# Kernel optimization log

Measured on AMD Instinct MI355X. Metric: run time of the kernel, lower is better.

## Reference

```python
import jax, jax.numpy as jnp
import numpy as np

RADIUS = 0.2
NSAMPLE = 32
NPOINT = 2048
EPS = 1e-5


def setup_inputs() -> dict:
    key = jax.random.key(0)
    ks = jax.random.split(key, 6)
    B, N, C = 8, 8192, 64
    xyz = jax.random.uniform(ks[0], (B, N, 3), dtype=jnp.float32)
    features = jax.random.normal(ks[1], (B, C, N), dtype=jnp.float32)
    W1 = jax.random.normal(ks[2], (64, 67), dtype=jnp.float32) * 0.1
    W2 = jax.random.normal(ks[3], (64, 64), dtype=jnp.float32) * 0.1
    W3 = jax.random.normal(ks[4], (128, 64), dtype=jnp.float32) * 0.1
    return {
        'xyz': xyz, 'features': features,
        'W1': W1, 'g1': jnp.ones((64,), jnp.float32), 'b1': jnp.zeros((64,), jnp.float32),
        'W2': W2, 'g2': jnp.ones((64,), jnp.float32), 'b2': jnp.zeros((64,), jnp.float32),
        'W3': W3, 'g3': jnp.ones((128,), jnp.float32), 'b3': jnp.zeros((128,), jnp.float32),
    }


def furthest_point_sample(xyz, npoint):
    # xyz: (B, N, 3) -> (B, npoint) int32 indices, first index is 0 (CUDA FPS convention)
    B, N, _ = xyz.shape
    idxs0 = jnp.zeros((B, npoint), dtype=jnp.int32)
    dists0 = jnp.full((B, N), 1e10, dtype=xyz.dtype)
    last0 = jnp.zeros((B,), dtype=jnp.int32)

    def body(i, state):
        idxs, dists, last = state
        last_pt = xyz[jnp.arange(B), last]                      # (B, 3)
        d = jnp.sum((xyz - last_pt[:, None, :]) ** 2, axis=-1)  # (B, N)
        dists = jnp.minimum(dists, d)
        nxt = jnp.argmax(dists, axis=-1).astype(jnp.int32)
        idxs = idxs.at[:, i].set(nxt)
        return (idxs, dists, nxt)

    idxs, _, _ = jax.lax.fori_loop(1, npoint, body, (idxs0, dists0, last0))
    return idxs


def ball_query(xyz, new_xyz, radius, nsample):
    # Returns (B, S, nsample) int32: first `nsample` points within radius of each
    # query center, padded with the first in-ball index (pointnet2 convention).
    N = xyz.shape[1]
    d2 = jnp.sum((new_xyz[:, :, None, :] - xyz[:, None, :, :]) ** 2, axis=-1)  # (B,S,N)
    key = jnp.where(d2 < radius * radius, jnp.arange(N, dtype=jnp.int32), N)
    neg_vals, _ = jax.lax.top_k(-key, nsample)   # k smallest keys = earliest in-ball indices
    cand = -neg_vals                             # (B, S, nsample)
    first = cand[..., :1]
    return jnp.where(cand < N, cand, first)


def reference(xyz, features, W1, g1, b1, W2, g2, b2, W3, g3, b3):
    B = xyz.shape[0]
    fps_idx = furthest_point_sample(xyz, NPOINT)              # (B, S)
    new_xyz = xyz[jnp.arange(B)[:, None], fps_idx]            # (B, S, 3)

    idx = ball_query(xyz, new_xyz, RADIUS, NSAMPLE)           # (B, S, ns)
    bb = jnp.arange(B)[:, None, None]
    grouped_xyz = xyz[bb, idx] - new_xyz[:, :, None, :]       # (B, S, ns, 3) relative coords
    grouped_f = features.transpose(0, 2, 1)[bb, idx]          # (B, S, ns, C)
    g = jnp.concatenate([grouped_xyz, grouped_f], axis=-1)    # (B, S, ns, 3+C)
    g = g.transpose(0, 3, 1, 2)                               # (B, 3+C, S, ns)

    for W, ga, be in ((W1, g1, b1), (W2, g2, b2), (W3, g3, b3)):
        h = jnp.einsum('oc,bcsn->bosn', W, g)                 # 1x1 conv
        mu = h.mean(axis=(0, 2, 3), keepdims=True)            # training-mode BN stats
        var = h.var(axis=(0, 2, 3), keepdims=True)
        h = (h - mu) / jnp.sqrt(var + EPS)
        g = jax.nn.relu(h * ga[None, :, None, None] + be[None, :, None, None])

    feats = g.max(axis=-1)                                    # (B, mlp[-1], S)
    return new_xyz, feats
```

## Files before the change

### kernel.cpp

```cpp
#include <hip/hip_runtime.h>
#include <hip/hip_bf16.h>
#include <stdint.h>

#define NB 8
#define NN 8192
#define NC 64
#define NS 2048
#define NK 32
#define NCOL (NB*NS*NK)

typedef float v2f __attribute__((ext_vector_type(2)));

__device__ __forceinline__ unsigned short f2bf(float x) {
    union { float f; unsigned u; } c; c.f = x;
    unsigned r = c.u + 0x7fffu + ((c.u >> 16) & 1u);
    return (unsigned short)(r >> 16);
}
__device__ __forceinline__ float bf2f(unsigned v16) {
    union { float f; unsigned u; } c; c.u = v16 << 16;
    return c.f;
}

template<int CTRL>
__device__ __forceinline__ unsigned long long dpp_max_u64(unsigned long long key) {
    int olo = __builtin_amdgcn_update_dpp(0, (int)(unsigned)key,        CTRL, 0xf, 0xf, true);
    int ohi = __builtin_amdgcn_update_dpp(0, (int)(unsigned)(key >> 32), CTRL, 0xf, 0xf, true);
    unsigned long long ok = ((unsigned long long)(unsigned)ohi << 32) | (unsigned)olo;
    return ok > key ? ok : key;
}
template<int CTRL>
__device__ __forceinline__ float dpp_add_f32(float x) {
    int o = __builtin_amdgcn_update_dpp(0, __float_as_int(x), CTRL, 0xf, 0xf, true);
    return x + __int_as_float(o);
}
template<int CTRL>
__device__ __forceinline__ float dpp_max_f32(float x) {
    int o = __builtin_amdgcn_update_dpp(__float_as_int(x), __float_as_int(x), CTRL, 0xf, 0xf, false);
    return fmaxf(x, __int_as_float(o));
}
template<int CTRL>
__device__ __forceinline__ float dpp_min_f32(float x) {
    int o = __builtin_amdgcn_update_dpp(__float_as_int(x), __float_as_int(x), CTRL, 0xf, 0xf, false);
    return fminf(x, __int_as_float(o));
}
template<int CTRL, int RM>
__device__ __forceinline__ unsigned dpp_add_u32(unsigned x) {
    int o = __builtin_amdgcn_update_dpp(0, (int)x, CTRL, RM, 0xf, true);
    return x + (unsigned)o;
}
__device__ __forceinline__ float wave_red_min(float x) {
    x = dpp_min_f32<0x111>(x); x = dpp_min_f32<0x112>(x);
    x = dpp_min_f32<0x114>(x); x = dpp_min_f32<0x118>(x);
    x = dpp_min_f32<0x142>(x); x = dpp_min_f32<0x143>(x);
    return __int_as_float(__builtin_amdgcn_readlane(__float_as_int(x), 63));
}
__device__ __forceinline__ float wave_red_max(float x) {
    x = dpp_max_f32<0x111>(x); x = dpp_max_f32<0x112>(x);
    x = dpp_max_f32<0x114>(x); x = dpp_max_f32<0x118>(x);
    x = dpp_max_f32<0x142>(x); x = dpp_max_f32<0x143>(x);
    return __int_as_float(__builtin_amdgcn_readlane(__float_as_int(x), 63));
}
__device__ __forceinline__ v2f relu2(v2f v) {
    v.x = fmaxf(v.x, 0.f); v.y = fmaxf(v.y, 0.f); return v;
}

__device__ __forceinline__ unsigned expand_bits10(unsigned v) {
    v = (v * 0x00010001u) & 0xFF0000FFu;
    v = (v * 0x00000101u) & 0x0F00F00Fu;
    v = (v * 0x00000011u) & 0xC30C30C3u;
    v = (v * 0x00000005u) & 0x49249249u;
    return v;
}
__global__ __launch_bounds__(1024) void sort_kernel(const float* __restrict__ xyz,
    float4* __restrict__ sorted)
{
    __shared__ unsigned cnt[2048];
    __shared__ unsigned codes[NN];
    __shared__ unsigned wsum[16];
    const int b = blockIdx.x;
    const int tid = threadIdx.x;
    const int w = tid >> 6;
    const int lane = tid & 63;
    const float* xb = xyz + (size_t)b * NN * 3;
    cnt[tid] = 0; cnt[tid + 1024] = 0;
    __syncthreads();
    for (int p = tid; p < NN; p += 1024) {
        float x = xb[3*p+0], y = xb[3*p+1], z = xb[3*p+2];
        int qx = (int)(x * 1024.f); qx = qx < 0 ? 0 : (qx > 1023 ? 1023 : qx);
        int qy = (int)(y * 1024.f); qy = qy < 0 ? 0 : (qy > 1023 ? 1023 : qy);
        int qz = (int)(z * 1024.f); qz = qz < 0 ? 0 : (qz > 1023 ? 1023 : qz);
        unsigned m = expand_bits10((unsigned)qx)
                   | (expand_bits10((unsigned)qy) << 1)
                   | (expand_bits10((unsigned)qz) << 2);
        unsigned bk = m >> 19;
        codes[p] = bk;
        atomicAdd(&cnt[bk], 1u);
    }
    __syncthreads();
    unsigned c0 = cnt[2*tid], c1 = cnt[2*tid+1];
    unsigned s = c0 + c1;
    unsigned v = s;
    v = dpp_add_u32<0x111, 0xf>(v);
    v = dpp_add_u32<0x112, 0xf>(v);
    v = dpp_add_u32<0x114, 0xf>(v);
    v = dpp_add_u32<0x118, 0xf>(v);
    v = dpp_add_u32<0x142, 0xa>(v);
    v = dpp_add_u32<0x143, 0xc>(v);
    if (lane == 63) wsum[w] = v;
    __syncthreads();
    unsigned wbase = 0;
#pragma unroll
    for (int j = 0; j < 15; ++j) {
        unsigned t = wsum[j];
        wbase += (j < w) ? t : 0u;
    }
    unsigned excl = wbase + v - s;
    cnt[2*tid]   = excl;
    cnt[2*tid+1] = excl + c0;
    __syncthreads();
    for (int p = tid; p < NN; p += 1024) {
        unsigned bk = codes[p];
        unsigned pos = atomicAdd(&cnt[bk], 1u);
        float4 o;
        o.x = xb[3*p+0]; o.y = xb[3*p+1]; o.z = xb[3*p+2];
        o.w = __int_as_float(p);
        sorted[(size_t)b * NN + pos] = o;
    }
}

__global__ __launch_bounds__(1024) void fps_kernel(const float* __restrict__ xyz,
    const float4* __restrict__ sorted,
    float* __restrict__ new_xyz, float* __restrict__ out_newxyz)
{
#pragma clang fp contract(off)
    const int b = blockIdx.x;
    const int tid = threadIdx.x;
    const int w = tid >> 6;
    const int lane = tid & 63;
    __shared__ float sx[NN], sy[NN], sz[NN];
    __shared__ float s_hist[NS * 3];
    __shared__ unsigned long long s_key[16];
    const float4* sp = sorted + (size_t)b * NN + (size_t)w * 512 + lane;
    v2f px[4], py[4], pz[4], dmin[4];
    unsigned plo[8];
    float bnx = 1e30f, bny = 1e30f, bnz = 1e30f;
    float bxx = -1e30f, bxy = -1e30f, bxz = -1e30f;
#pragma unroll
    for (int m = 0; m < 4; ++m) {
        float4 a = sp[128*m];
        float4 c = sp[128*m + 64];
        px[m].x = a.x; px[m].y = c.x;
        py[m].x = a.y; py[m].y = c.y;
        pz[m].x = a.z; pz[m].y = c.z;
        dmin[m].x = 1e10f; dmin[m].y = 1e10f;
        int ia = __float_as_int(a.w), ic = __float_as_int(c.w);
        plo[2*m]   = ~(unsigned)ia;
        plo[2*m+1] = ~(unsigned)ic;
        sx[ia] = a.x; sy[ia] = a.y; sz[ia] = a.z;
        sx[ic] = c.x; sy[ic] = c.y; sz[ic] = c.z;
        bnx = fminf(bnx, fminf(a.x, c.x)); bxx = fmaxf(bxx, fmaxf(a.x, c.x));
        bny = fminf(bny, fminf(a.y, c.y)); bxy = fmaxf(bxy, fmaxf(a.y, c.y));
        bnz = fminf(bnz, fminf(a.z, c.z)); bxz = fmaxf(bxz, fmaxf(a.z, c.z));
    }
    bnx = wave_red_min(bnx); bny = wave_red_min(bny); bnz = wave_red_min(bnz);
    bxx = wave_red_max(bxx); bxy = wave_red_max(bxy); bxz = wave_red_max(bxz);

    const float* xb = xyz + (size_t)b * NN * 3;
    float lx = xb[0], ly = xb[1], lz = xb[2];
    if (tid == 0) { s_hist[0] = lx; s_hist[1] = ly; s_hist[2] = lz; }
    float ckv = 1e30f;
    unsigned cklo = 0u;
    __syncthreads();

    for (int i = 1; i < NS; ++i) {
        float cdx = fmaxf(fmaxf(bnx - lx, lx - bxx), 0.f);
        float cdy = fmaxf(fmaxf(bny - ly, ly - bxy), 0.f);
        float cdz = fmaxf(fmaxf(bnz - lz, lz - bxz), 0.f);
        float lb = (cdx*cdx + cdy*cdy) + cdz*cdz;
        if (!(lb >= ckv)) {
            v2f l2x; l2x.x = lx; l2x.y = lx;
            v2f l2y; l2y.x = ly; l2y.y = ly;
            v2f l2z; l2z.x = lz; l2z.y = lz;
            unsigned long long best = 0ull;
#pragma unroll
            for (int m = 0; m < 4; ++m) {
                v2f dx = px[m] - l2x;
                v2f dy = py[m] - l2y;
                v2f dz = pz[m] - l2z;
                v2f d = (dx*dx + dy*dy) + dz*dz;
                v2f dm;
                dm.x = fminf(dmin[m].x, d.x);
                dm.y = fminf(dmin[m].y, d.y);
                dmin[m] = dm;
                unsigned long long k0 =
                    ((unsigned long long)__float_as_uint(dm.x) << 32) | plo[2*m];
                unsigned long long k1 =
                    ((unsigned long long)__float_as_uint(dm.y) << 32) | plo[2*m+1];
                if (k0 > best) best = k0;
                if (k1 > best) best = k1;
            }
            best = dpp_max_u64<0x111>(best);
            best = dpp_max_u64<0x112>(best);
            best = dpp_max_u64<0x114>(best);
            best = dpp_max_u64<0x118>(best);
            best = dpp_max_u64<0x142>(best);
            best = dpp_max_u64<0x143>(best);
            ckv  = __uint_as_float((unsigned)__builtin_amdgcn_readlane((int)(best >> 32), 63));
            cklo = (unsigned)__builtin_amdgcn_readlane((int)(best & 0xffffffffull), 63);
        }
        if (lane == 0)
            s_key[w] = ((unsigned long long)__float_as_uint(ckv) << 32) | cklo;
        __syncthreads();
        if (w == 0) {
            unsigned long long k = s_key[lane & 15];
            k = dpp_max_u64<0x111>(k);
            k = dpp_max_u64<0x112>(k);
            k = dpp_max_u64<0x114>(k);
            k = dpp_max_u64<0x118>(k);
            int lo15 = __builtin_amdgcn_readlane((int)(k & 0xffffffffull), 15);
            int ix = ~lo15;
            float nx = sx[ix], ny = sy[ix], nz = sz[ix];
            if (lane == 0) {
                s_hist[3*i+0] = nx; s_hist[3*i+1] = ny; s_hist[3*i+2] = nz;
            }
        }
        __syncthreads();
        lx = s_hist[3*i+0]; ly = s_hist[3*i+1]; lz = s_hist[3*i+2];
    }
    __syncthreads();
    float* nw = new_xyz + (size_t)b * NS * 3;
    float* ow = out_newxyz + (size_t)b * NS * 3;
    for (int t = tid; t < NS * 3; t += 1024) {
        float v = s_hist[t];
        nw[t] = v; ow[t] = v;
    }
}

__global__ __launch_bounds__(256) void transpose_kernel(const float* __restrict__ f,
    float* __restrict__ ft)
{
    __shared__ float tile[64][65];
    int b = blockIdx.y;
    int p0 = blockIdx.x * 64;
    for (int k = threadIdx.x; k < 64*64; k += 256) {
        int c = k >> 6, p = k & 63;
        tile[c][p] = f[((size_t)b * NC + c) * NN + p0 + p];
    }
    __syncthreads();
    for (int k = threadIdx.x; k < 64*64; k += 256) {
        int p = k >> 6, c = k & 63;
        ft[((size_t)b * NN + p0 + p) * NC + c] = tile[c][p];
    }
}

__global__ __launch_bounds__(256) void ballquery_kernel(const float* __restrict__ xyz,
    const float* __restrict__ new_xyz, int* __restrict__ idx)
{
#pragma clang fp contract(off)
    const int q = blockIdx.x * 4 + (threadIdx.x >> 6);
    const int lane = threadIdx.x & 63;
    const int b = q >> 11;
    const float r2 = (float)(0.2 * 0.2);
    const float* xb = xyz + (size_t)b * NN * 3;
    const float* nx = new_xyz + (size_t)q * 3;
    float qx = nx[0], qy = nx[1], qz = nx[2];
    int cnt = 0, first = -1;
    int* out = idx + (size_t)q * NK;
    for (int base = 0; base < NN; base += 64) {
        int p = base + lane;
        float x = xb[p*3+0], y = xb[p*3+1], z = xb[p*3+2];
        float dx = qx - x, dy = qy - y, dz = qz - z;
        float d2 = (dx*dx + dy*dy) + dz*dz;
        bool in = d2 < r2;
        unsigned long long m = __ballot(in);
        if (m) {
            if (first < 0) first = base + __builtin_ctzll(m);
            if (in) {
                int rank = cnt + __popcll(m & ((1ull << lane) - 1ull));
                if (rank < NK) out[rank] = p;
            }
            cnt += __popcll(m);
            if (cnt >= NK) break;
        }
    }
    for (int k = cnt + lane; k < NK; k += 64) out[k] = first;
}

__global__ __launch_bounds__(256, 2) void layer1_kernel(const float* __restrict__ xyz,
    const float* __restrict__ new_xyz, const int* __restrict__ idx,
    const float* __restrict__ ft, const float* __restrict__ W1,
    unsigned short* __restrict__ h1)
{
    const int col = blockIdx.x * 256 + threadIdx.x;
    const int b = col >> 16;
    const int s = (col >> 5) & 2047;
    const int p = idx[col];
    v2f g[34];
    float* gf = (float*)g;
    {
        const float* nx = new_xyz + ((size_t)(b * NS + s)) * 3;
        const float* xp = xyz + ((size_t)(b * NN + p)) * 3;
        gf[0] = xp[0] - nx[0]; gf[1] = xp[1] - nx[1]; gf[2] = xp[2] - nx[2];
    }
    const float4* fp = (const float4*)(ft + ((size_t)(b * NN + p)) * NC);
#pragma unroll
    for (int c4 = 0; c4 < 16; ++c4) {
        float4 v = fp[c4];
        gf[3 + 4*c4 + 0] = v.x; gf[3 + 4*c4 + 1] = v.y;
        gf[3 + 4*c4 + 2] = v.z; gf[3 + 4*c4 + 3] = v.w;
    }
    gf[67] = 0.f;
    uint4* dst = (uint4*)(h1 + (size_t)col * 64);
#pragma unroll
    for (int half = 0; half < 2; ++half) {
        float h[32];
#pragma unroll 4
        for (int o16 = 0; o16 < 32; ++o16) {
            const float* w = W1 + (half*32 + o16) * 67;
            v2f acc; acc.x = 0.f; acc.y = 0.f;
#pragma unroll
            for (int k = 0; k < 33; ++k) {
                v2f wv; wv.x = w[2*k]; wv.y = w[2*k+1];
                acc = wv * g[k] + acc;
            }
            h[o16] = fmaf(w[66], gf[66], acc.x + acc.y);
        }
#pragma unroll
        for (int k = 0; k < 4; ++k) {
            uint4 v;
            v.x = (unsigned)f2bf(h[8*k+0]) | ((unsigned)f2bf(h[8*k+1]) << 16);
            v.y = (unsigned)f2bf(h[8*k+2]) | ((unsigned)f2bf(h[8*k+3]) << 16);
            v.z = (unsigned)f2bf(h[8*k+4]) | ((unsigned)f2bf(h[8*k+5]) << 16);
            v.w = (unsigned)f2bf(h[8*k+6]) | ((unsigned)f2bf(h[8*k+7]) << 16);
            dst[half*4 + k] = v;
        }
    }
}

__global__ __launch_bounds__(256) void stats_kernel(const unsigned short* __restrict__ h,
    float* __restrict__ sums)
{
    __shared__ float ls[64], lq[64];
    const int tid = threadIdx.x;
    if (tid < 64) { ls[tid] = 0.f; lq[tid] = 0.f; }
    __syncthreads();
    float s[8] = {0,0,0,0,0,0,0,0}, q[8] = {0,0,0,0,0,0,0,0};
    const int gt = blockIdx.x * 256 + tid;
    const int G = gridDim.x * 256;
    const uint4* src = (const uint4*)h;
    const int nvec = NCOL * 8;
    for (int i = gt; i < nvec; i += G) {
        uint4 v = src[i];
        float f0 = bf2f(v.x & 0xffffu), f1 = bf2f(v.x >> 16);
        float f2 = bf2f(v.y & 0xffffu), f3 = bf2f(v.y >> 16);
        float f4 = bf2f(v.z & 0xffffu), f5 = bf2f(v.z >> 16);
        float f6 = bf2f(v.w & 0xffffu), f7 = bf2f(v.w >> 16);
        s[0] += f0; q[0] = fmaf(f0, f0, q[0]);
        s[1] += f1; q[1] = fmaf(f1, f1, q[1]);
        s[2] += f2; q[2] = fmaf(f2, f2, q[2]);
        s[3] += f3; q[3] = fmaf(f3, f3, q[3]);
        s[4] += f4; q[4] = fmaf(f4, f4, q[4]);
        s[5] += f5; q[5] = fmaf(f5, f5, q[5]);
        s[6] += f6; q[6] = fmaf(f6, f6, q[6]);
        s[7] += f7; q[7] = fmaf(f7, f7, q[7]);
    }
    const int obase = (tid & 7) * 8;
#pragma unroll
    for (int j = 0; j < 8; ++j) {
        atomicAdd(&ls[obase + j], s[j]);
        atomicAdd(&lq[obase + j], q[j]);
    }
    __syncthreads();
    if (tid < 64) {
        atomicAdd(&sums[tid*2+0], ls[tid]);
        atomicAdd(&sums[tid*2+1], lq[tid]);
    }
}

__global__ void finalize_kernel(const float* __restrict__ sums,
    const float* __restrict__ gamma, const float* __restrict__ beta,
    float* __restrict__ ab, int nch)
{
    int c = threadIdx.x;
    if (c < nch) {
        const float invM = 1.0f / 524288.0f;
        float mu = sums[c*2] * invM;
        float var = sums[c*2+1] * invM - mu * mu;
        float a = gamma[c] / sqrtf(var + 1e-5f);
        ab[c] = a;
        ab[nch + c] = fmaf(-mu, a, beta[c]);
    }
}

__global__ __launch_bounds__(256, 2) void layer2_kernel(const unsigned short* __restrict__ h1,
    const float* __restrict__ ab1, const float* __restrict__ W2,
    unsigned short* __restrict__ h2)
{
    const int col = blockIdx.x * 256 + threadIdx.x;
    const uint4* src = (const uint4*)(h1 + (size_t)col * 64);
    v2f g[32];
    float* gf = (float*)g;
#pragma unroll
    for (int k = 0; k < 8; ++k) {
        uint4 v = src[k];
        gf[8*k+0] = bf2f(v.x & 0xffffu); gf[8*k+1] = bf2f(v.x >> 16);
        gf[8*k+2] = bf2f(v.y & 0xffffu); gf[8*k+3] = bf2f(v.y >> 16);
        gf[8*k+4] = bf2f(v.z & 0xffffu); gf[8*k+5] = bf2f(v.z >> 16);
        gf[8*k+6] = bf2f(v.w & 0xffffu); gf[8*k+7] = bf2f(v.w >> 16);
    }
    const v2f* a2 = (const v2f*)ab1;
    const v2f* b2 = (const v2f*)(ab1 + 64);
#pragma unroll
    for (int k = 0; k < 32; ++k)
        g[k] = relu2(a2[k] * g[k] + b2[k]);
    uint4* dst = (uint4*)(h2 + (size_t)col * 64);
#pragma unroll
    for (int half = 0; half < 2; ++half) {
        float h[32];
#pragma unroll 4
        for (int o16 = 0; o16 < 32; ++o16) {
            const float* w = W2 + ((half*32 + o16) << 6);
            v2f acc; acc.x = 0.f; acc.y = 0.f;
#pragma unroll
            for (int k = 0; k < 32; ++k) {
                v2f wv; wv.x = w[2*k]; wv.y = w[2*k+1];
                acc = wv * g[k] + acc;
            }
            h[o16] = acc.x + acc.y;
        }
#pragma unroll
        for (int k = 0; k < 4; ++k) {
            uint4 v;
            v.x = (unsigned)f2bf(h[8*k+0]) | ((unsigned)f2bf(h[8*k+1]) << 16);
            v.y = (unsigned)f2bf(h[8*k+2]) | ((unsigned)f2bf(h[8*k+3]) << 16);
            v.z = (unsigned)f2bf(h[8*k+4]) | ((unsigned)f2bf(h[8*k+5]) << 16);
            v.w = (unsigned)f2bf(h[8*k+6]) | ((unsigned)f2bf(h[8*k+7]) << 16);
            dst[half*4 + k] = v;
        }
    }
}

__global__ __launch_bounds__(256, 2) void layer3_kernel(const unsigned short* __restrict__ h2,
    const float* __restrict__ ab2, const float* __restrict__ W3,
    float* __restrict__ hmax, float* __restrict__ hmin, float* __restrict__ sums3)
{
    __shared__ float ls[128], lq[128];
    const int tid = threadIdx.x;
    if (tid < 128) { ls[tid] = 0.f; lq[tid] = 0.f; }
    __syncthreads();
    const int col = blockIdx.x * 256 + tid;
    const int q = col >> 5;
    const uint4* src = (const uint4*)(h2 + (size_t)col * 64);
    v2f g[32];
    float* gf = (float*)g;
#pragma unroll
    for (int k = 0; k < 8; ++k) {
        uint4 v = src[k];
        gf[8*k+0] = bf2f(v.x & 0xffffu); gf[8*k+1] = bf2f(v.x >> 16);
        gf[8*k+2] = bf2f(v.y & 0xffffu); gf[8*k+3] = bf2f(v.y >> 16);
        gf[8*k+4] = bf2f(v.z & 0xffffu); gf[8*k+5] = bf2f(v.z >> 16);
        gf[8*k+6] = bf2f(v.w & 0xffffu); gf[8*k+7] = bf2f(v.w >> 16);
    }
    const v2f* a2 = (const v2f*)ab2;
    const v2f* b2 = (const v2f*)(ab2 + 64);
#pragma unroll
    for (int k = 0; k < 32; ++k)
        g[k] = relu2(a2[k] * g[k] + b2[k]);
    const bool leader = ((tid & 31) == 31);
#pragma unroll 2
    for (int o = 0; o < 128; ++o) {
        const float* w = W3 + (o << 6);
        v2f acc; acc.x = 0.f; acc.y = 0.f;
#pragma unroll
        for (int k = 0; k < 32; ++k) {
            v2f wv; wv.x = w[2*k]; wv.y = w[2*k+1];
            acc = wv * g[k] + acc;
        }
        float hv = acc.x + acc.y;
        float sm = hv, sq = hv*hv, mx = hv, mn = hv;
        sm = dpp_add_f32<0x111>(sm); sq = dpp_add_f32<0x111>(sq);
        mx = dpp_max_f32<0x111>(mx); mn = dpp_min_f32<0x111>(mn);
        sm = dpp_add_f32<0x112>(sm); sq = dpp_add_f32<0x112>(sq);
        mx = dpp_max_f32<0x112>(mx); mn = dpp_min_f32<0x112>(mn);
        sm = dpp_add_f32<0x114>(sm); sq = dpp_add_f32<0x114>(sq);
        mx = dpp_max_f32<0x114>(mx); mn = dpp_min_f32<0x114>(mn);
        sm = dpp_add_f32<0x118>(sm); sq = dpp_add_f32<0x118>(sq);
        mx = dpp_max_f32<0x118>(mx); mn = dpp_min_f32<0x118>(mn);
        sm = dpp_add_f32<0x142>(sm); sq = dpp_add_f32<0x142>(sq);
        mx = dpp_max_f32<0x142>(mx); mn = dpp_min_f32<0x142>(mn);
        if (leader) {
            hmax[(size_t)o * 16384 + q] = mx;
            hmin[(size_t)o * 16384 + q] = mn;
            atomicAdd(&ls[o], sm);
            atomicAdd(&lq[o], sq);
        }
    }
    __syncthreads();
    if (tid < 128) {
        atomicAdd(&sums3[tid*2+0], ls[tid]);
        atomicAdd(&sums3[tid*2+1], lq[tid]);
    }
}

__global__ __launch_bounds__(256) void final_kernel(const float* __restrict__ hmax,
    const float* __restrict__ hmin, const float* __restrict__ ab3,
    float* __restrict__ out)
{
    const int t = blockIdx.x * 256 + threadIdx.x;
    const int s = t & 2047;
    const int o = (t >> 11) & 127;
    const int b = t >> 18;
    const int q = (b << 11) + s;
    float a = ab3[o], c = ab3[128 + o];
    float h = (a >= 0.f) ? hmax[(size_t)o * 16384 + q] : hmin[(size_t)o * 16384 + q];
    out[t] = fmaxf(fmaf(a, h, c), 0.f);
}

extern "C" void kernel_launch(void* const* d_in, const int* in_sizes, int n_in,
                              void* d_out, int out_size, void* d_ws, size_t ws_size,
                              hipStream_t stream) {
    (void)in_sizes; (void)n_in; (void)out_size; (void)ws_size;
    const float* xyz      = (const float*)d_in[0];
    const float* features = (const float*)d_in[1];
    const float* W1 = (const float*)d_in[2];
    const float* g1 = (const float*)d_in[3];
    const float* b1 = (const float*)d_in[4];
    const float* W2 = (const float*)d_in[5];
    const float* g2 = (const float*)d_in[6];
    const float* b2 = (const float*)d_in[7];
    const float* W3 = (const float*)d_in[8];
    const float* g3 = (const float*)d_in[9];
    const float* b3 = (const float*)d_in[10];

    char* ws = (char*)d_ws;
    float*          new_xyz = (float*)(ws + 0);
    int*            idx     = (int*)(ws + 196608);
    float*          ft      = (float*)(ws + 2293760);
    unsigned short* h1      = (unsigned short*)(ws + 19070976);
    unsigned short* h2      = (unsigned short*)(ws + 86179840);
    float*          hmax    = (float*)(ws + 153288704);
    float*          hmin    = (float*)(ws + 161677312);
    float*          sums    = (float*)(ws + 170065920);
    float*          ab      = (float*)(ws + 170067968);
    float* sums1 = sums;        float* ab1 = ab;
    float* sums2 = sums + 128;  float* ab2 = ab + 128;
    float* sums3 = sums + 256;  float* ab3 = ab + 256;

    float4* sorted = (float4*)h1;

    float* out_newxyz = (float*)d_out;
    float* out_feats  = (float*)d_out + 49152;

    hipMemsetAsync(sums, 0, 2048, stream);

    sort_kernel<<<NB, 1024, 0, stream>>>(xyz, sorted);
    fps_kernel<<<NB, 1024, 0, stream>>>(xyz, sorted, new_xyz, out_newxyz);
    transpose_kernel<<<dim3(NN/64, NB), 256, 0, stream>>>(features, ft);
    ballquery_kernel<<<(NB*NS)/4, 256, 0, stream>>>(xyz, new_xyz, idx);
    layer1_kernel<<<NCOL/256, 256, 0, stream>>>(xyz, new_xyz, idx, ft, W1, h1);
    stats_kernel<<<1024, 256, 0, stream>>>(h1, sums1);
    finalize_kernel<<<1, 128, 0, stream>>>(sums1, g1, b1, ab1, 64);
    layer2_kernel<<<NCOL/256, 256, 0, stream>>>(h1, ab1, W2, h2);
    stats_kernel<<<1024, 256, 0, stream>>>(h2, sums2);
    finalize_kernel<<<1, 128, 0, stream>>>(sums2, g2, b2, ab2, 64);
    layer3_kernel<<<NCOL/256, 256, 0, stream>>>(h2, ab2, W3, hmax, hmin, sums3);
    finalize_kernel<<<1, 128, 0, stream>>>(sums3, g3, b3, ab3, 128);
    final_kernel<<<(NB*128*NS)/256, 256, 0, stream>>>(hmax, hmin, ab3, out_feats);
}
```

Baseline: 2.112 ms.

## Use shared atomicMax with triple-buffered slots to drop one FPS barrier

Each wave now publishes its candidate key with a 64-bit LDS atomicMax into a rotating slot instead of writing per-wave keys that wave 0 then reduces. After a single barrier every thread reads the winning key and fetches the next point's coordinates itself. This removes the second __syncthreads and the serial wave-0 reduction from each of the 2047 FPS iterations. The cost is LDS atomic contention across 16 waves and a triple-buffer scheme whose slot reset has to stay correctly ordered with later readers.

```diff
diff --git a/kernel.cpp b/kernel.cpp
--- a/kernel.cpp
+++ b/kernel.cpp
@@ -139,7 +139,7 @@
     const int lane = tid & 63;
     __shared__ float sx[NN], sy[NN], sz[NN];
     __shared__ float s_hist[NS * 3];
-    __shared__ unsigned long long s_key[16];
+    __shared__ unsigned long long s_slot[3];
     const float4* sp = sorted + (size_t)b * NN + (size_t)w * 512 + lane;
     v2f px[4], py[4], pz[4], dmin[4];
     unsigned plo[8];
@@ -167,12 +167,17 @@
 
     const float* xb = xyz + (size_t)b * NN * 3;
     float lx = xb[0], ly = xb[1], lz = xb[2];
-    if (tid == 0) { s_hist[0] = lx; s_hist[1] = ly; s_hist[2] = lz; }
+    if (tid == 0) {
+        s_hist[0] = lx; s_hist[1] = ly; s_hist[2] = lz;
+        s_slot[0] = 0ull; s_slot[1] = 0ull; s_slot[2] = 0ull;
+    }
     float ckv = 1e30f;
     unsigned cklo = 0u;
     __syncthreads();
 
+    int cur = 1, nxt = 2;
     for (int i = 1; i < NS; ++i) {
+        if (tid == 0) s_slot[nxt] = 0ull;
         float cdx = fmaxf(fmaxf(bnx - lx, lx - bxx), 0.f);
         float cdy = fmaxf(fmaxf(bny - ly, ly - bxy), 0.f);
         float cdz = fmaxf(fmaxf(bnz - lz, lz - bxz), 0.f);
@@ -209,23 +214,17 @@
             cklo = (unsigned)__builtin_amdgcn_readlane((int)(best & 0xffffffffull), 63);
         }
         if (lane == 0)
-            s_key[w] = ((unsigned long long)__float_as_uint(ckv) << 32) | cklo;
+            atomicMax(&s_slot[cur],
+                      ((unsigned long long)__float_as_uint(ckv) << 32) | cklo);
         __syncthreads();
-        if (w == 0) {
-            unsigned long long k = s_key[lane & 15];
-            k = dpp_max_u64<0x111>(k);
-            k = dpp_max_u64<0x112>(k);
-            k = dpp_max_u64<0x114>(k);
-            k = dpp_max_u64<0x118>(k);
-            int lo15 = __builtin_amdgcn_readlane((int)(k & 0xffffffffull), 15);
-            int ix = ~lo15;
-            float nx = sx[ix], ny = sy[ix], nz = sz[ix];
-            if (lane == 0) {
-                s_hist[3*i+0] = nx; s_hist[3*i+1] = ny; s_hist[3*i+2] = nz;
-            }
-        }
-        __syncthreads();
-        lx = s_hist[3*i+0]; ly = s_hist[3*i+1]; lz = s_hist[3*i+2];
+        const unsigned long long k = s_slot[cur];
+        const int ix = ~(int)(unsigned)(k & 0xffffffffull);
+        lx = sx[ix]; ly = sy[ix]; lz = sz[ix];
+        if (tid == 0) {
+            s_hist[3*i+0] = lx; s_hist[3*i+1] = ly; s_hist[3*i+2] = lz;
+        }
+        cur = nxt;
+        nxt = nxt + 1; if (nxt == 3) nxt = 0;
     }
     __syncthreads();
     float* nw = new_xyz + (size_t)b * NS * 3;
```

Result: faster. 2.039 ms (-3.5%).
